# Kernel tuning notes

Hardware: AMD Instinct MI355X
Metric: run time of the kernel (lower is better)

The kernel has to match this reference:

```python
import jax, jax.numpy as jnp
import numpy as np

K_WAVE = 15.0  # wavenumber k from source
EPS_R = 1e-8   # epsilon in dr/dn denominator from source


def bessel_j1(x):
    # Numerical-Recipes rational/asymptotic approximation of J1(x).
    ax = jnp.abs(x)
    y = x * x
    num = x * (72362614232.0 + y * (-7895059235.0 + y * (242396853.1 + y * (-2972611.439 + y * (15704.48260 + y * (-30.16036606))))))
    den = 144725228442.0 + y * (2300535178.0 + y * (18583304.74 + y * (99447.43394 + y * (376.9991397 + y))))
    small = num / den
    axs = jnp.maximum(ax, 1e-20)
    z = 8.0 / axs
    y2 = z * z
    xx = axs - 2.356194491
    p1 = 1.0 + y2 * (0.183105e-2 + y2 * (-0.3516396496e-4 + y2 * (0.2457520174e-5 + y2 * (-0.240337019e-6))))
    p2 = 0.04687499995 + y2 * (-0.2002690873e-3 + y2 * (0.8449199096e-5 + y2 * (-0.88228987e-6 + y2 * 0.105787412e-6)))
    large = jnp.sqrt(0.636619772 / axs) * (jnp.cos(xx) * p1 - z * jnp.sin(xx) * p2) * jnp.sign(x)
    return jnp.where(ax < 8.0, small, large)


def bessel_y1(x):
    # Numerical-Recipes approximation of Y1(x), x > 0.
    xs = jnp.maximum(x, 1e-12)
    y = xs * xs
    num = xs * (-4.900604943e13 + y * (1.275274390e13 + y * (-5.153438139e11 + y * (7.349264551e9 + y * (-4.237922726e7 + y * 8.511937935e4)))))
    den = 2.499580570e14 + y * (4.244419664e12 + y * (3.733650367e10 + y * (2.245904002e8 + y * (1.020426050e6 + y * (3.549632885e3 + y)))))
    small = num / den + 0.636619772 * (bessel_j1(xs) * jnp.log(xs) - 1.0 / xs)
    z = 8.0 / xs
    y2 = z * z
    xx = xs - 2.356194491
    p1 = 1.0 + y2 * (0.183105e-2 + y2 * (-0.3516396496e-4 + y2 * (0.2457520174e-5 + y2 * (-0.240337019e-6))))
    p2 = 0.04687499995 + y2 * (-0.2002690873e-3 + y2 * (0.8449199096e-5 + y2 * (-0.88228987e-6 + y2 * 0.105787412e-6)))
    large = jnp.sqrt(0.636619772 / xs) * (jnp.sin(xx) * p1 + z * jnp.cos(xx) * p2)
    return jnp.where(xs < 8.0, small, large)


def _mlp(pts, W1, b1, W2, b2, W3, b3, W4, b4, W5, b5):
    h = jnp.tanh(pts @ W1 + b1)
    h = jnp.tanh(h @ W2 + b2)
    h = jnp.tanh(h @ W3 + b3)
    h = jnp.tanh(h @ W4 + b4)
    return (h @ W5 + b5)[:, 0]  # [M]


def setup_inputs() -> dict:
    key = jax.random.key(0)
    ks = jax.random.split(key, 12)
    N = 1024            # points per side (source uses 50)
    P = 16384           # query points
    H = 50              # hidden width (source default)
    cords = np.linspace(0.0001, 0.9999, N, dtype=np.float32)
    z = np.zeros(N, dtype=np.float32)
    o = np.ones(N, dtype=np.float32)
    top = np.stack([cords, o], 1)
    bottom = np.stack([cords, z], 1)
    left = np.stack([z, cords], 1)
    right = np.stack([o, cords], 1)
    boundary_points = jnp.asarray(np.concatenate([top, bottom, left, right], 0))  # [4N,2]
    nrm = np.concatenate([
        np.stack([z, o], 1),    # top normal (0,1)
        np.stack([z, -o], 1),   # bottom (0,-1)
        np.stack([-o, z], 1),   # left (-1,0)
        np.stack([o, z], 1),    # right (1,0)
    ], 0)
    normals = jnp.asarray(nrm)
    dy = jnp.float32(1.0 / (N - 1))
    points = jax.random.uniform(ks[0], (P, 2), dtype=jnp.float32)
    def lin(k, fin, fout):
        lim = np.sqrt(6.0 / (fin + fout)).astype(np.float32)
        return jax.random.uniform(k, (fin, fout), minval=-lim, maxval=lim, dtype=jnp.float32)
    return {
        'points': points,
        'boundary_points': boundary_points,
        'normals': normals,
        'dy': dy,
        'W1': lin(ks[1], 2, H), 'b1': jnp.zeros((H,), jnp.float32),
        'W2': lin(ks[2], H, H), 'b2': jnp.zeros((H,), jnp.float32),
        'W3': lin(ks[3], H, H), 'b3': jnp.zeros((H,), jnp.float32),
        'W4': lin(ks[4], H, H), 'b4': jnp.zeros((H,), jnp.float32),
        'W5': lin(ks[5], H, 1), 'b5': jnp.zeros((1,), jnp.float32),
    }


def reference(points, boundary_points, normals, dy, W1, b1, W2, b2, W3, b3, W4, b4, W5, b5):
    # density values on the boundary from the MLP
    h_vals = _mlp(boundary_points, W1, b1, W2, b2, W3, b3, W4, b4, W5, b5)  # [M]
    # pairwise geometry: [P, M, 2]
    diff = points[:, None, :] - boundary_points[None, :, :]
    r = jnp.sqrt(jnp.sum(diff * diff, axis=-1))               # [P, M]
    dr_dn = jnp.sum(diff * normals[None, :, :], axis=-1) / (r + EPS_R)
    # Re[-(i/4)*k*H1^{(1)}(k r)] = (k/4)*Y1(k r); output is the real part only,
    # so the J1 (imaginary) component never contributes to the returned value.
    y1 = jax.lax.stop_gradient(bessel_y1(K_WAVE * r))  # hankel term is detached in torch (numpy round-trip)
    green_real = 0.25 * K_WAVE * y1 * dr_dn                   # [P, M]
    u_real = jnp.sum(green_real * h_vals[None, :], axis=-1) * dy  # [P]
    return u_real
```

## Files before the change

kernel.cpp:

```cpp
#include <hip/hip_runtime.h>
#include <math.h>

#define H 50
#define TPB 256
#define K_WAVE 15.0f
#define NSIDE 1024
#define STEP (0.9998f / 1023.0f)
#define NB_MLP 1024
#define N_TAB 2304
#define NB_TAB 9
#define IDX_BASE 5952

__device__ float y1_f(float x) {
    float inv_x = __fdividef(1.0f, x);
    float y = x * x;
    float nj = fmaf(y, -30.16036606f, 15704.48260f);
    nj = fmaf(y, nj, -2972611.439f);
    nj = fmaf(y, nj, 242396853.1f);
    nj = fmaf(y, nj, -7895059235.0f);
    nj = fmaf(y, nj, 72362614232.0f);
    nj *= x;
    float dj = y + 376.9991397f;
    dj = fmaf(y, dj, 99447.43394f);
    dj = fmaf(y, dj, 18583304.74f);
    dj = fmaf(y, dj, 2300535178.0f);
    dj = fmaf(y, dj, 144725228442.0f);
    float j1 = __fdividef(nj, dj);
    float ny1 = fmaf(y, 8.511937935e4f, -4.237922726e7f);
    ny1 = fmaf(y, ny1, 7.349264551e9f);
    ny1 = fmaf(y, ny1, -5.153438139e11f);
    ny1 = fmaf(y, ny1, 1.275274390e13f);
    ny1 = fmaf(y, ny1, -4.900604943e13f);
    ny1 *= x;
    float dy1 = y + 3.549632885e3f;
    dy1 = fmaf(y, dy1, 1.020426050e6f);
    dy1 = fmaf(y, dy1, 2.245904002e8f);
    dy1 = fmaf(y, dy1, 3.733650367e10f);
    dy1 = fmaf(y, dy1, 4.244419664e12f);
    dy1 = fmaf(y, dy1, 2.499580570e14f);
    float y1_small = __fdividef(ny1, dy1) + 0.636619772f * (j1 * __logf(x) - inv_x);
    float z = 8.0f * inv_x;
    float y2 = z * z;
    float xx = x - 2.356194491f;
    float p1 = fmaf(y2, -0.240337019e-6f, 0.2457520174e-5f);
    p1 = fmaf(y2, p1, -0.3516396496e-4f);
    p1 = fmaf(y2, p1, 0.183105e-2f);
    p1 = fmaf(y2, p1, 1.0f);
    float p2 = fmaf(y2, 0.105787412e-6f, -0.88228987e-6f);
    p2 = fmaf(y2, p2, 0.8449199096e-5f);
    p2 = fmaf(y2, p2, -0.2002690873e-3f);
    p2 = fmaf(y2, p2, 0.04687499995f);
    float s, c;
    __sincosf(xx, &s, &c);
    float y1_large = sqrtf(0.636619772f * inv_x) * fmaf(s, p1, z * c * p2);
    return (x < 8.0f) ? y1_small : y1_large;
}

__device__ float G_of_u_node(int i) {
    float u = __uint_as_float((unsigned)(IDX_BASE + i) << 17);
    float x = K_WAVE * sqrtf(u);
    return __fdividef(x * y1_f(x), u);
}

__global__ __launch_bounds__(256) void prep_kernel(
    const float* __restrict__ bp,
    const float* __restrict__ W1, const float* __restrict__ b1,
    const float* __restrict__ W2, const float* __restrict__ b2,
    const float* __restrict__ W3, const float* __restrict__ b3,
    const float* __restrict__ W4, const float* __restrict__ b4,
    const float* __restrict__ W5, const float* __restrict__ b5,
    const float* __restrict__ dyp,
    float* __restrict__ h_out, float2* __restrict__ tab, int M)
{
    if (blockIdx.x >= NB_MLP) {
        int i = (blockIdx.x - NB_MLP) * 256 + threadIdx.x;
        if (i < N_TAB) {
            float g0 = G_of_u_node(i);
            float g1 = G_of_u_node(i + 1);
            tab[i] = make_float2(g0, (g1 - g0) * (1.0f / 131072.0f));
        }
        return;
    }
    __shared__ float ha[4][56];
    __shared__ float hb[4][56];
    int wave = threadIdx.x >> 6;
    int j = threadIdx.x & 63;
    int m = blockIdx.x * 4 + wave;
    if (m >= M) return;
    float px = bp[2 * m], py = bp[2 * m + 1];

    if (j < H) {
        ha[wave][j] = tanhf(fmaf(px, W1[j], fmaf(py, W1[H + j], b1[j])));
    }
    __syncthreads();
    if (j < H) {
        float s = b2[j];
        #pragma unroll
        for (int i = 0; i < H; ++i) s = fmaf(ha[wave][i], W2[i * H + j], s);
        hb[wave][j] = tanhf(s);
    }
    __syncthreads();
    if (j < H) {
        float s = b3[j];
        #pragma unroll
        for (int i = 0; i < H; ++i) s = fmaf(hb[wave][i], W3[i * H + j], s);
        ha[wave][j] = tanhf(s);
    }
    __syncthreads();
    if (j < H) {
        float s = b4[j];
        #pragma unroll
        for (int i = 0; i < H; ++i) s = fmaf(ha[wave][i], W4[i * H + j], s);
        hb[wave][j] = tanhf(s);
    }
    __syncthreads();
    if (j == 0) {
        float s = b5[0];
        #pragma unroll
        for (int i = 0; i < H; ++i) s = fmaf(hb[wave][i], W5[i], s);
        h_out[m] = s * (0.25f * dyp[0]);
    }
}

__global__ __launch_bounds__(TPB, 8) void pair_kernel(
    const float* __restrict__ pts,
    const float* __restrict__ hs,
    const float2* __restrict__ tab,
    float* __restrict__ out, int P)
{
    __shared__ float2 lt[N_TAB];
    for (int i = threadIdx.x; i < N_TAB; i += TPB) lt[i] = tab[i];
    __syncthreads();

    int wave = threadIdx.x >> 6;
    int lane = threadIdx.x & 63;
    int p0 = blockIdx.x * 8 + wave * 2;

    float pxa = pts[2 * p0],     pya = pts[2 * p0 + 1];
    float pxb = pts[2 * p0 + 2], pyb = pts[2 * p0 + 3];

    float tota = 0.0f, totb = 0.0f;
    float base = fmaf((float)lane, STEP, 0.0001f);

    #pragma unroll
    for (int side = 0; side < 4; ++side) {
        float va, vb, wa, wb, sgn;
        if (side == 0)      { va = pxa; wa = pya - 1.0f; vb = pxb; wb = pyb - 1.0f; sgn =  1.0f; }
        else if (side == 1) { va = pxa; wa = pya;        vb = pxb; wb = pyb;        sgn = -1.0f; }
        else if (side == 2) { va = pya; wa = pxa;        vb = pyb; wb = pxb;        sgn = -1.0f; }
        else                { va = pya; wa = pxa - 1.0f; vb = pyb; wb = pxb - 1.0f; sgn =  1.0f; }
        float w2a = wa * wa;
        float w2b = wb * wb;
        float d0a = va - base;
        float d0b = vb - base;
        const float* hp = hs + side * NSIDE + lane;
        float acca = 0.0f, accb = 0.0f;
        #pragma unroll 4
        for (int t = 0; t < NSIDE / 64; ++t) {
            float hm = hp[t * 64];
            float ct = (float)(t * 64) * STEP;
            {
                float dx = d0a - ct;
                float u = fmaxf(fmaf(dx, dx, w2a), 6.0e-11f);
                unsigned b = __float_as_uint(u);
                int   i  = (int)(b >> 17) - IDX_BASE;
                float f  = (float)(b & 0x1FFFFu);
                float2 gs = lt[i];
                acca = fmaf(fmaf(f, gs.y, gs.x), hm, acca);
            }
            {
                float dx = d0b - ct;
                float u = fmaxf(fmaf(dx, dx, w2b), 6.0e-11f);
                unsigned b = __float_as_uint(u);
                int   i  = (int)(b >> 17) - IDX_BASE;
                float f  = (float)(b & 0x1FFFFu);
                float2 gs = lt[i];
                accb = fmaf(fmaf(f, gs.y, gs.x), hm, accb);
            }
        }
        tota = fmaf(acca, wa * sgn, tota);
        totb = fmaf(accb, wb * sgn, totb);
    }

    #pragma unroll
    for (int off = 32; off >= 1; off >>= 1) {
        tota += __shfl_xor(tota, off, 64);
        totb += __shfl_xor(totb, off, 64);
    }
    if (lane == 0) {
        out[p0]     = tota;
        out[p0 + 1] = totb;
    }
}

extern "C" void kernel_launch(void* const* d_in, const int* in_sizes, int n_in,
                              void* d_out, int out_size, void* d_ws, size_t ws_size,
                              hipStream_t stream) {
    const float* pts = (const float*)d_in[0];
    const float* bp  = (const float*)d_in[1];
    const float* dyp = (const float*)d_in[3];
    const float* W1 = (const float*)d_in[4];  const float* b1 = (const float*)d_in[5];
    const float* W2 = (const float*)d_in[6];  const float* b2 = (const float*)d_in[7];
    const float* W3 = (const float*)d_in[8];  const float* b3 = (const float*)d_in[9];
    const float* W4 = (const float*)d_in[10]; const float* b4 = (const float*)d_in[11];
    const float* W5 = (const float*)d_in[12]; const float* b5 = (const float*)d_in[13];

    int P = in_sizes[0] / 2;
    int M = in_sizes[1] / 2;

    float*  hs  = (float*)d_ws;
    float2* tab = (float2*)((char*)d_ws + (size_t)M * 4);

    prep_kernel<<<dim3(NB_MLP + NB_TAB), dim3(256), 0, stream>>>(
        bp, W1, b1, W2, b2, W3, b3, W4, b4, W5, b5, dyp, hs, tab, M);

    pair_kernel<<<dim3(P / 8), dim3(TPB), 0, stream>>>(
        pts, hs, tab, (float*)d_out, P);
}
```

Before: 108.2 us.

## Pair opposite boundary sides and simplify table lookup via scaled-exponent indexing

The pair kernel now handles two parallel sides together. Each shares the same dx term, so one squared distance feeds two table lookups, and the h values are interleaved as float2 loads. The table lookup is rewritten: u is scaled by 2^-92 so the table byte offset comes straight from the shifted float bits, and the table stores c0/c1 so the integer bits act as the interpolant without masking or subtracting a base. The MLP prep also drops its __syncthreads barriers (relying on per-wave locality), splits the dot-product accumulators, and does the last layer with a wave shuffle. Correctness depends on the scaled bit pattern landing in the table range and on float precision of (float)bu for the interpolation.

```diff
diff --git a/kernel.cpp b/kernel.cpp
--- a/kernel.cpp
+++ b/kernel.cpp
@@ -7,9 +7,10 @@
 #define NSIDE 1024
 #define STEP (0.9998f / 1023.0f)
 #define NB_MLP 1024
-#define N_TAB 2304
-#define NB_TAB 9
-#define IDX_BASE 5952
+#define N_TAB 2368
+#define NB_TAB 10
+#define IDX_SHIFT 5888
+#define SC 0x1p-92f
 
 __device__ float y1_f(float x) {
     float inv_x = __fdividef(1.0f, x);
@@ -56,8 +57,8 @@
     return (x < 8.0f) ? y1_small : y1_large;
 }
 
-__device__ float G_of_u_node(int i) {
-    float u = __uint_as_float((unsigned)(IDX_BASE + i) << 17);
+__device__ float G_of_u_node(int idx) {
+    float u = __uint_as_float((unsigned)(IDX_SHIFT + idx) << 17);
     float x = K_WAVE * sqrtf(u);
     return __fdividef(x * y1_f(x), u);
 }
@@ -70,14 +71,20 @@
     const float* __restrict__ W4, const float* __restrict__ b4,
     const float* __restrict__ W5, const float* __restrict__ b5,
     const float* __restrict__ dyp,
-    float* __restrict__ h_out, float2* __restrict__ tab, int M)
+    float* __restrict__ hs2, float2* __restrict__ tab, int M)
 {
     if (blockIdx.x >= NB_MLP) {
         int i = (blockIdx.x - NB_MLP) * 256 + threadIdx.x;
         if (i < N_TAB) {
-            float g0 = G_of_u_node(i);
-            float g1 = G_of_u_node(i + 1);
-            tab[i] = make_float2(g0, (g1 - g0) * (1.0f / 131072.0f));
+            if (i < 64) {
+                tab[i] = make_float2(0.0f, 0.0f);
+            } else {
+                float g0 = G_of_u_node(i);
+                float g1 = G_of_u_node(i + 1);
+                float c1 = (g1 - g0) * (1.0f / 131072.0f);
+                float c0 = g0 - c1 * (float)(i << 17);
+                tab[i] = make_float2(c0, c1);
+            }
         }
         return;
     }
@@ -92,39 +99,46 @@
     if (j < H) {
         ha[wave][j] = tanhf(fmaf(px, W1[j], fmaf(py, W1[H + j], b1[j])));
     }
-    __syncthreads();
-    if (j < H) {
-        float s = b2[j];
+    if (j < H) {
+        float s0 = b2[j], s1 = 0.0f;
         #pragma unroll
-        for (int i = 0; i < H; ++i) s = fmaf(ha[wave][i], W2[i * H + j], s);
-        hb[wave][j] = tanhf(s);
-    }
-    __syncthreads();
-    if (j < H) {
-        float s = b3[j];
+        for (int i = 0; i < H; i += 2) {
+            s0 = fmaf(ha[wave][i],     W2[i * H + j],       s0);
+            s1 = fmaf(ha[wave][i + 1], W2[(i + 1) * H + j], s1);
+        }
+        hb[wave][j] = tanhf(s0 + s1);
+    }
+    if (j < H) {
+        float s0 = b3[j], s1 = 0.0f;
         #pragma unroll
-        for (int i = 0; i < H; ++i) s = fmaf(hb[wave][i], W3[i * H + j], s);
-        ha[wave][j] = tanhf(s);
-    }
-    __syncthreads();
-    if (j < H) {
-        float s = b4[j];
+        for (int i = 0; i < H; i += 2) {
+            s0 = fmaf(hb[wave][i],     W3[i * H + j],       s0);
+            s1 = fmaf(hb[wave][i + 1], W3[(i + 1) * H + j], s1);
+        }
+        ha[wave][j] = tanhf(s0 + s1);
+    }
+    float v = 0.0f;
+    if (j < H) {
+        float s0 = b4[j], s1 = 0.0f;
         #pragma unroll
-        for (int i = 0; i < H; ++i) s = fmaf(ha[wave][i], W4[i * H + j], s);
-        hb[wave][j] = tanhf(s);
-    }
-    __syncthreads();
+        for (int i = 0; i < H; i += 2) {
+            s0 = fmaf(ha[wave][i],     W4[i * H + j],       s0);
+            s1 = fmaf(ha[wave][i + 1], W4[(i + 1) * H + j], s1);
+        }
+        v = tanhf(s0 + s1) * W5[j];
+    }
+    #pragma unroll
+    for (int off = 32; off >= 1; off >>= 1) v += __shfl_xor(v, off, 64);
     if (j == 0) {
-        float s = b5[0];
-        #pragma unroll
-        for (int i = 0; i < H; ++i) s = fmaf(hb[wave][i], W5[i], s);
-        h_out[m] = s * (0.25f * dyp[0]);
+        float s = (v + b5[0]) * (0.25f * dyp[0]);
+        int side = m >> 10, x = m & (NSIDE - 1);
+        hs2[(((side >> 1) << 10) + x) * 2 + (side & 1)] = s;
     }
 }
 
 __global__ __launch_bounds__(TPB, 8) void pair_kernel(
     const float* __restrict__ pts,
-    const float* __restrict__ hs,
+    const float2* __restrict__ hs2,
     const float2* __restrict__ tab,
     float* __restrict__ out, int P)
 {
@@ -143,43 +157,59 @@
     float base = fmaf((float)lane, STEP, 0.0001f);
 
     #pragma unroll
-    for (int side = 0; side < 4; ++side) {
-        float va, vb, wa, wb, sgn;
-        if (side == 0)      { va = pxa; wa = pya - 1.0f; vb = pxb; wb = pyb - 1.0f; sgn =  1.0f; }
-        else if (side == 1) { va = pxa; wa = pya;        vb = pxb; wb = pyb;        sgn = -1.0f; }
-        else if (side == 2) { va = pya; wa = pxa;        vb = pyb; wb = pxb;        sgn = -1.0f; }
-        else                { va = pya; wa = pxa - 1.0f; vb = pyb; wb = pxb - 1.0f; sgn =  1.0f; }
-        float w2a = wa * wa;
-        float w2b = wb * wb;
+    for (int sp = 0; sp < 2; ++sp) {
+        float va  = sp ? pya : pxa;
+        float vb  = sp ? pyb : pxb;
+        float wea = sp ? pxa : pya - 1.0f;
+        float web = sp ? pxb : pyb - 1.0f;
+        float woa = sp ? pxa - 1.0f : pya;
+        float wob = sp ? pxb - 1.0f : pyb;
+        float sea = sp ? -wea : wea;
+        float seb = sp ? -web : web;
+        float soa = sp ? woa : -woa;
+        float sob = sp ? wob : -wob;
+        float w2ea = wea * wea, w2eb = web * web;
+        float w2oa = woa * woa, w2ob = wob * wob;
+
+        const float2* hp2 = hs2 + sp * NSIDE + lane;
         float d0a = va - base;
         float d0b = vb - base;
-        const float* hp = hs + side * NSIDE + lane;
-        float acca = 0.0f, accb = 0.0f;
-        #pragma unroll 4
+        float aae = 0.0f, aao = 0.0f, abe = 0.0f, abo = 0.0f;
+        #pragma unroll 2
         for (int t = 0; t < NSIDE / 64; ++t) {
-            float hm = hp[t * 64];
+            float2 hm = hp2[t * 64];
             float ct = (float)(t * 64) * STEP;
-            {
-                float dx = d0a - ct;
-                float u = fmaxf(fmaf(dx, dx, w2a), 6.0e-11f);
-                unsigned b = __float_as_uint(u);
-                int   i  = (int)(b >> 17) - IDX_BASE;
-                float f  = (float)(b & 0x1FFFFu);
-                float2 gs = lt[i];
-                acca = fmaf(fmaf(f, gs.y, gs.x), hm, acca);
-            }
-            {
-                float dx = d0b - ct;
-                float u = fmaxf(fmaf(dx, dx, w2b), 6.0e-11f);
-                unsigned b = __float_as_uint(u);
-                int   i  = (int)(b >> 17) - IDX_BASE;
-                float f  = (float)(b & 0x1FFFFu);
-                float2 gs = lt[i];
-                accb = fmaf(fmaf(f, gs.y, gs.x), hm, accb);
-            }
-        }
-        tota = fmaf(acca, wa * sgn, tota);
-        totb = fmaf(accb, wb * sgn, totb);
+            float dxa = d0a - ct;  float d2a = dxa * dxa;
+            float dxb = d0b - ct;  float d2b = dxb * dxb;
+            {
+                float u = fmaxf(d2a + w2ea, 6.0e-11f);
+                unsigned bu = __float_as_uint(u * SC);
+                float2 gs = *(const float2*)((const char*)lt + ((bu >> 14) & ~7u));
+                aae = fmaf(fmaf((float)bu, gs.y, gs.x), hm.x, aae);
+            }
+            {
+                float u = fmaxf(d2a + w2oa, 6.0e-11f);
+                unsigned bu = __float_as_uint(u * SC);
+                float2 gs = *(const float2*)((const char*)lt + ((bu >> 14) & ~7u));
+                aao = fmaf(fmaf((float)bu, gs.y, gs.x), hm.y, aao);
+            }
+            {
+                float u = fmaxf(d2b + w2eb, 6.0e-11f);
+                unsigned bu = __float_as_uint(u * SC);
+                float2 gs = *(const float2*)((const char*)lt + ((bu >> 14) & ~7u));
+                abe = fmaf(fmaf((float)bu, gs.y, gs.x), hm.x, abe);
+            }
+            {
+                float u = fmaxf(d2b + w2ob, 6.0e-11f);
+                unsigned bu = __float_as_uint(u * SC);
+                float2 gs = *(const float2*)((const char*)lt + ((bu >> 14) & ~7u));
+                abo = fmaf(fmaf((float)bu, gs.y, gs.x), hm.y, abo);
+            }
+        }
+        tota = fmaf(aae, sea, tota);
+        tota = fmaf(aao, soa, tota);
+        totb = fmaf(abe, seb, totb);
+        totb = fmaf(abo, sob, totb);
     }
 
     #pragma unroll
@@ -208,12 +238,12 @@
     int P = in_sizes[0] / 2;
     int M = in_sizes[1] / 2;
 
-    float*  hs  = (float*)d_ws;
-    float2* tab = (float2*)((char*)d_ws + (size_t)M * 4);
+    float*  hs2 = (float*)d_ws;
+    float2* tab = (float2*)((char*)d_ws + 2 * NSIDE * 8);
 
     prep_kernel<<<dim3(NB_MLP + NB_TAB), dim3(256), 0, stream>>>(
-        bp, W1, b1, W2, b2, W3, b3, W4, b4, W5, b5, dyp, hs, tab, M);
+        bp, W1, b1, W2, b2, W3, b3, W4, b4, W5, b5, dyp, hs2, tab, M);
 
     pair_kernel<<<dim3(P / 8), dim3(TPB), 0, stream>>>(
-        pts, hs, tab, (float*)d_out, P);
-}
+        pts, (const float2*)hs2, tab, (float*)d_out, P);
+}
```

New measurement: 104.3 us. -3.6%, faster.
